# Optimization experiments

Hardware: AMD Instinct MI355X
Metric: run time of the kernel (lower is better)

## Reference

```python
import jax, jax.numpy as jnp
import numpy as np

N_MBED = 384
HEAD_SIZE = 64

def setup_inputs() -> dict:
    key = jax.random.key(0)
    kx, kq, kk, kv = jax.random.split(key, 4)
    B, T = 128, 256
    x = jax.random.normal(kx, (B, T, N_MBED), dtype=jnp.float32)
    # torch nn.Linear(n_mbed, head_size, bias=False): y = x @ W^T, W:[head_size, n_mbed].
    # We store the transposed weight [n_mbed, head_size] so y = x @ W.
    s = 1.0 / np.sqrt(N_MBED)
    Wq = jax.random.uniform(kq, (N_MBED, HEAD_SIZE), jnp.float32, -s, s)
    Wk = jax.random.uniform(kk, (N_MBED, HEAD_SIZE), jnp.float32, -s, s)
    Wv = jax.random.uniform(kv, (N_MBED, HEAD_SIZE), jnp.float32, -s, s)
    return {"x": x, "Wq": Wq, "Wk": Wk, "Wv": Wv}

def reference(x, Wq, Wk, Wv):
    B, T, C = x.shape  # C = n_mbed = 384
    q = x @ Wq  # [B,T,H]
    k = x @ Wk
    v = x @ Wv
    # Faithful to source: wei = k @ q^T, scaled by C**-0.5 (C = n_mbed, not head_size)
    wei = jnp.einsum('bth,bsh->bts', k, q) * (C ** -0.5)  # [B,T,T]
    mask = jnp.tril(jnp.ones((T, T), dtype=bool))
    wei = jnp.where(mask, wei, -jnp.inf)
    wei = jax.nn.softmax(wei, axis=-1)
    # dropout omitted (eval mode / identity)
    out = jnp.einsum('bts,bsh->bth', wei, v)  # [B,T,H]
    return out
```

## Files before the change

### kernel.cpp

```cpp
#include <hip/hip_runtime.h>
#include <hip/hip_bf16.h>
#include <math.h>

constexpr int kB = 128;
constexpr int kT = 256;
constexpr int kC = 384;
constexpr int kH = 64;

using bf16x8 = __attribute__((ext_vector_type(8))) short;
using f32x4  = __attribute__((ext_vector_type(4))) float;

union BF4 { short4 s; __hip_bfloat162 h[2]; };

__device__ inline short4 cvt4(float4 a) {
    BF4 u;
    u.h[0] = __float22bfloat162_rn(float2{a.x, a.y});
    u.h[1] = __float22bfloat162_rn(float2{a.z, a.w});
    return u.s;
}
__device__ inline short bf1(float f) {
    __hip_bfloat16 h = __float2bfloat16(f);
    return *(short*)&h;
}

__global__ void prep_kernel(const float* __restrict__ Wq,
                            const float* __restrict__ Wk,
                            const float* __restrict__ Wv,
                            __hip_bfloat16* __restrict__ Wt) {
    int idx = blockIdx.x * 256 + threadIdx.x;
    int n = idx / kC, c = idx % kC;
    int w = n >> 6, h = n & 63;
    const float* W = (w == 0) ? Wq : (w == 1) ? Wk : Wv;
    float val = W[c * kH + h];
    if (w == 1) val *= 0.051031036307982884f;
    Wt[idx] = __float2bfloat16(val);
}

__global__ __launch_bounds__(256, 4) void proj_kernel(
    const float* __restrict__ x, const __hip_bfloat16* __restrict__ Wt,
    short* __restrict__ Qg, short* __restrict__ Kg, short* __restrict__ VTg)
{
    __shared__ short As[2][64 * 36];
    __shared__ short Bs[2][192 * 36];

    const int bid = blockIdx.x;
    const int b   = bid & 127;
    const int q4  = bid >> 7;
    const int row0 = b * kT + q4 * 64;

    const int tid  = threadIdx.x;
    const int wave = tid >> 6, lane = tid & 63;
    const int m16  = lane & 15, quad = lane >> 4;
    const short* wt = (const short*)Wt;

    const int arow = tid >> 2, acol = (tid & 3) * 8;
    const float* xr = x + (size_t)(row0 + arow) * kC;

    float4 la[2]; bf16x8 lb[3];
    auto glod = [&](int k0) {
        la[0] = *(const float4*)(xr + k0 + acol);
        la[1] = *(const float4*)(xr + k0 + acol + 4);
#pragma unroll
        for (int p = 0; p < 3; ++p) {
            int c = tid + 256 * p, n = c >> 2, kk = (c & 3) * 8;
            lb[p] = *(const bf16x8*)(wt + (size_t)n * kC + k0 + kk);
        }
    };
    auto swr = [&](int d) {
        *(short4*)&As[d][arow * 36 + acol]     = cvt4(la[0]);
        *(short4*)&As[d][arow * 36 + acol + 4] = cvt4(la[1]);
#pragma unroll
        for (int p = 0; p < 3; ++p) {
            int c = tid + 256 * p, n = c >> 2, kk = (c & 3) * 8;
            *(bf16x8*)&Bs[d][n * 36 + kk] = lb[p];
        }
    };

    f32x4 acc[4][3];
#pragma unroll
    for (int mt = 0; mt < 4; ++mt)
#pragma unroll
        for (int j = 0; j < 3; ++j) acc[mt][j] = f32x4{0.f, 0.f, 0.f, 0.f};

    glod(0);
    swr(0);
    __syncthreads();

    for (int s = 0; s < 12; ++s) {
        const int d = s & 1;
        if (s < 11) glod((s + 1) * 32);

        bf16x8 af[4];
#pragma unroll
        for (int mt = 0; mt < 4; ++mt)
            af[mt] = *(const bf16x8*)&As[d][(mt * 16 + m16) * 36 + quad * 8];
#pragma unroll
        for (int j = 0; j < 3; ++j) {
            const bf16x8 bfr =
                *(const bf16x8*)&Bs[d][((wave * 3 + j) * 16 + m16) * 36 + quad * 8];
#pragma unroll
            for (int mt = 0; mt < 4; ++mt)
                acc[mt][j] = __builtin_amdgcn_mfma_f32_16x16x32_bf16(
                    af[mt], bfr, acc[mt][j], 0, 0, 0);
        }

        if (s < 11) swr(d ^ 1);
        __syncthreads();
    }

#pragma unroll
    for (int mt = 0; mt < 4; ++mt) {
        const int mrow = mt * 16 + quad * 4;
#pragma unroll
        for (int j = 0; j < 3; ++j) {
            const int nt = wave * 3 + j;
            const int w  = nt >> 2;
            const int h  = (nt & 3) * 16 + m16;
            if (w == 2) {
                float4 f = make_float4(acc[mt][j][0], acc[mt][j][1],
                                       acc[mt][j][2], acc[mt][j][3]);
                *(short4*)&VTg[((size_t)b * kH + h) * kT + q4 * 64 + mrow] = cvt4(f);
            } else {
                short* G = (w == 1) ? Kg : Qg;
#pragma unroll
                for (int r = 0; r < 4; ++r)
                    G[((size_t)b * kT + q4 * 64 + mrow + r) * kH + h] = bf1(acc[mt][j][r]);
            }
        }
    }
}

__global__ __launch_bounds__(256, 4) void attn_kernel(
    const short* __restrict__ Qg, const short* __restrict__ Kg,
    const short* __restrict__ VTg, float* __restrict__ out)
{
    __shared__ short Pbuf[4][16 * 72];

    const int bid = blockIdx.x;
    const int b   = ((bid >> 5) << 3) | (bid & 7);
    const int qi  = (bid >> 3) & 3;

    const int tid  = threadIdx.x;
    const int wave = tid >> 6, lane = tid & 63;
    const int m16  = lane & 15, quad = lane >> 4;
    const int trow0 = qi * 64 + wave * 16;

    const short* Qb = Qg  + (size_t)b * kT * kH;
    const short* Kb = Kg  + (size_t)b * kT * kH;
    const short* Vb = VTg + (size_t)b * kH * kT;
    short* Pb = Pbuf[wave];

    const bf16x8 ka0 = *(const bf16x8*)&Kb[(trow0 + m16) * kH + quad * 8];
    const bf16x8 ka1 = *(const bf16x8*)&Kb[(trow0 + m16) * kH + quad * 8 + 32];

    f32x4 O[4];
    float m_[4], l_[4];
#pragma unroll
    for (int i = 0; i < 4; ++i) {
        O[i] = f32x4{0.f, 0.f, 0.f, 0.f};
        m_[i] = -INFINITY; l_[i] = 0.f;
    }

    for (int i = 0; i <= qi; ++i) {
        const bool diag = (i == qi);
        const int jmax = diag ? wave : 3;

        f32x4 S[4];
        const f32x4 Z = f32x4{0.f, 0.f, 0.f, 0.f};
#pragma unroll
        for (int j = 0; j < 4; ++j) {
            if (j <= jmax) {
                const int s = i * 64 + j * 16 + m16;
                bf16x8 qb0 = *(const bf16x8*)&Qb[s * kH + quad * 8];
                bf16x8 qb1 = *(const bf16x8*)&Qb[s * kH + quad * 8 + 32];
                S[j] = __builtin_amdgcn_mfma_f32_16x16x32_bf16(ka0, qb0, Z, 0, 0, 0);
                S[j] = __builtin_amdgcn_mfma_f32_16x16x32_bf16(ka1, qb1, S[j], 0, 0, 0);
            }
        }
        if (diag) {
#pragma unroll
            for (int r = 0; r < 4; ++r)
                if (m16 > quad * 4 + r) S[jmax][r] = -INFINITY;
        }

        float P[4][4];
#pragma unroll
        for (int j = 0; j < 4; ++j)
#pragma unroll
            for (int r = 0; r < 4; ++r) P[j][r] = 0.f;
#pragma unroll
        for (int r = 0; r < 4; ++r) {
            float rm = -INFINITY;
#pragma unroll
            for (int j = 0; j < 4; ++j)
                if (j <= jmax) rm = fmaxf(rm, S[j][r]);
            rm = fmaxf(rm, __shfl_xor(rm, 1, 64));
            rm = fmaxf(rm, __shfl_xor(rm, 2, 64));
            rm = fmaxf(rm, __shfl_xor(rm, 4, 64));
            rm = fmaxf(rm, __shfl_xor(rm, 8, 64));
            const float mn = fmaxf(m_[r], rm);
            const float al = __expf(m_[r] - mn);
            m_[r] = mn;
            float rs = 0.f;
#pragma unroll
            for (int j = 0; j < 4; ++j) {
                if (j <= jmax) { P[j][r] = __expf(S[j][r] - mn); rs += P[j][r]; }
            }
            rs += __shfl_xor(rs, 1, 64);
            rs += __shfl_xor(rs, 2, 64);
            rs += __shfl_xor(rs, 4, 64);
            rs += __shfl_xor(rs, 8, 64);
            l_[r] = l_[r] * al + rs;
            O[0][r] *= al; O[1][r] *= al; O[2][r] *= al; O[3][r] *= al;
        }

#pragma unroll
        for (int j = 0; j < 4; ++j)
#pragma unroll
            for (int r = 0; r < 4; ++r)
                Pb[(quad * 4 + r) * 72 + j * 16 + m16] = bf1(P[j][r]);
        bf16x8 pf0 = *(const bf16x8*)&Pb[m16 * 72 + quad * 8];
        bf16x8 pf1 = *(const bf16x8*)&Pb[m16 * 72 + quad * 8 + 32];

#pragma unroll
        for (int ht = 0; ht < 4; ++ht) {
            bf16x8 vb0 = *(const bf16x8*)&Vb[(ht * 16 + m16) * kT + i * 64 + quad * 8];
            bf16x8 vb1 = *(const bf16x8*)&Vb[(ht * 16 + m16) * kT + i * 64 + quad * 8 + 32];
            O[ht] = __builtin_amdgcn_mfma_f32_16x16x32_bf16(pf0, vb0, O[ht], 0, 0, 0);
            O[ht] = __builtin_amdgcn_mfma_f32_16x16x32_bf16(pf1, vb1, O[ht], 0, 0, 0);
        }
    }

#pragma unroll
    for (int r = 0; r < 4; ++r) {
        const float inv = 1.f / l_[r];
        const size_t row = (size_t)(b * kT + trow0 + quad * 4 + r);
#pragma unroll
        for (int ht = 0; ht < 4; ++ht)
            out[row * kH + ht * 16 + m16] = O[ht][r] * inv;
    }
}

extern "C" void kernel_launch(void* const* d_in, const int* in_sizes, int n_in,
                              void* d_out, int out_size, void* d_ws, size_t ws_size,
                              hipStream_t stream) {
    const float* x  = (const float*)d_in[0];
    const float* Wq = (const float*)d_in[1];
    const float* Wk = (const float*)d_in[2];
    const float* Wv = (const float*)d_in[3];
    float* out = (float*)d_out;

    short* base = (short*)d_ws;
    __hip_bfloat16* Wt = (__hip_bfloat16*)base;
    short* Qg  = base + 73728;
    short* Kg  = Qg + (size_t)kB * kT * kH;
    short* VTg = Kg + (size_t)kB * kT * kH;

    prep_kernel<<<(192 * kC) / 256, 256, 0, stream>>>(Wq, Wk, Wv, Wt);
    proj_kernel<<<dim3(512), 256, 0, stream>>>(x, Wt, Qg, Kg, VTg);
    attn_kernel<<<dim3(512), 256, 0, stream>>>(Qg, Kg, VTg, out);
}
```

Before: 122.1 us.

## Transpose QK^T MFMA so softmax rows reduce within lanes, prefetch V

The QK^T MFMA operands are swapped so each lane holds one query row's scores across its four accumulator registers. Row max and row sum then reduce mostly within a lane, with two cross-quad shuffles instead of four shuffles per register, and online-softmax state shrinks to one scalar per lane. The rescale factor and final normalizer are broadcast back to the output layout with shuffles. The P tile is now written as packed bf16 pairs, V fragments are loaded before the QK phase to hide latency, and s_setprio raises wave priority around the MFMA blocks. The layout swap touches the masking, reduction and output paths, so any index mistake would break correctness.

```diff
diff --git a/kernel.cpp b/kernel.cpp
--- a/kernel.cpp
+++ b/kernel.cpp
@@ -154,86 +154,110 @@
     const bf16x8 ka1 = *(const bf16x8*)&Kb[(trow0 + m16) * kH + quad * 8 + 32];
 
     f32x4 O[4];
-    float m_[4], l_[4];
-#pragma unroll
-    for (int i = 0; i < 4; ++i) {
-        O[i] = f32x4{0.f, 0.f, 0.f, 0.f};
-        m_[i] = -INFINITY; l_[i] = 0.f;
-    }
+#pragma unroll
+    for (int i = 0; i < 4; ++i) O[i] = f32x4{0.f, 0.f, 0.f, 0.f};
+    float m_ = -INFINITY, l_ = 0.f;
 
     for (int i = 0; i <= qi; ++i) {
         const bool diag = (i == qi);
         const int jmax = diag ? wave : 3;
 
+        bf16x8 vb[4][2];
+#pragma unroll
+        for (int ht = 0; ht < 4; ++ht) {
+            vb[ht][0] = *(const bf16x8*)&Vb[(ht * 16 + m16) * kT + i * 64 + quad * 8];
+            vb[ht][1] = *(const bf16x8*)&Vb[(ht * 16 + m16) * kT + i * 64 + quad * 8 + 32];
+        }
+
         f32x4 S[4];
         const f32x4 Z = f32x4{0.f, 0.f, 0.f, 0.f};
+        __builtin_amdgcn_s_setprio(1);
 #pragma unroll
         for (int j = 0; j < 4; ++j) {
             if (j <= jmax) {
                 const int s = i * 64 + j * 16 + m16;
                 bf16x8 qb0 = *(const bf16x8*)&Qb[s * kH + quad * 8];
                 bf16x8 qb1 = *(const bf16x8*)&Qb[s * kH + quad * 8 + 32];
-                S[j] = __builtin_amdgcn_mfma_f32_16x16x32_bf16(ka0, qb0, Z, 0, 0, 0);
-                S[j] = __builtin_amdgcn_mfma_f32_16x16x32_bf16(ka1, qb1, S[j], 0, 0, 0);
-            }
-        }
+                S[j] = __builtin_amdgcn_mfma_f32_16x16x32_bf16(qb0, ka0, Z, 0, 0, 0);
+                S[j] = __builtin_amdgcn_mfma_f32_16x16x32_bf16(qb1, ka1, S[j], 0, 0, 0);
+            }
+        }
+        __builtin_amdgcn_s_setprio(0);
         if (diag) {
 #pragma unroll
             for (int r = 0; r < 4; ++r)
-                if (m16 > quad * 4 + r) S[jmax][r] = -INFINITY;
-        }
+                if (quad * 4 + r > m16) S[jmax][r] = -INFINITY;
+        }
+
+        float rm = -INFINITY;
+#pragma unroll
+        for (int j = 0; j < 4; ++j)
+            if (j <= jmax)
+#pragma unroll
+                for (int r = 0; r < 4; ++r) rm = fmaxf(rm, S[j][r]);
+        rm = fmaxf(rm, __shfl_xor(rm, 16, 64));
+        rm = fmaxf(rm, __shfl_xor(rm, 32, 64));
+
+        const float mn = fmaxf(m_, rm);
+        const float al = __expf(m_ - mn);
+        m_ = mn;
 
         float P[4][4];
 #pragma unroll
         for (int j = 0; j < 4; ++j)
 #pragma unroll
             for (int r = 0; r < 4; ++r) P[j][r] = 0.f;
-#pragma unroll
-        for (int r = 0; r < 4; ++r) {
-            float rm = -INFINITY;
-#pragma unroll
-            for (int j = 0; j < 4; ++j)
-                if (j <= jmax) rm = fmaxf(rm, S[j][r]);
-            rm = fmaxf(rm, __shfl_xor(rm, 1, 64));
-            rm = fmaxf(rm, __shfl_xor(rm, 2, 64));
-            rm = fmaxf(rm, __shfl_xor(rm, 4, 64));
-            rm = fmaxf(rm, __shfl_xor(rm, 8, 64));
-            const float mn = fmaxf(m_[r], rm);
-            const float al = __expf(m_[r] - mn);
-            m_[r] = mn;
-            float rs = 0.f;
-#pragma unroll
-            for (int j = 0; j < 4; ++j) {
-                if (j <= jmax) { P[j][r] = __expf(S[j][r] - mn); rs += P[j][r]; }
-            }
-            rs += __shfl_xor(rs, 1, 64);
-            rs += __shfl_xor(rs, 2, 64);
-            rs += __shfl_xor(rs, 4, 64);
-            rs += __shfl_xor(rs, 8, 64);
-            l_[r] = l_[r] * al + rs;
-            O[0][r] *= al; O[1][r] *= al; O[2][r] *= al; O[3][r] *= al;
-        }
+        float rs = 0.f;
+#pragma unroll
+        for (int j = 0; j < 4; ++j) {
+            if (j <= jmax) {
+#pragma unroll
+                for (int r = 0; r < 4; ++r) {
+                    P[j][r] = __expf(S[j][r] - mn);
+                    rs += P[j][r];
+                }
+            }
+        }
+        rs += __shfl_xor(rs, 16, 64);
+        rs += __shfl_xor(rs, 32, 64);
+        l_ = l_ * al + rs;
+
+        float albc[4];
+#pragma unroll
+        for (int r = 0; r < 4; ++r)
+            albc[r] = __shfl(al, (quad << 4) | (quad * 4 + r), 64);
+#pragma unroll
+        for (int ht = 0; ht < 4; ++ht)
+#pragma unroll
+            for (int r = 0; r < 4; ++r) O[ht][r] *= albc[r];
 
 #pragma unroll
         for (int j = 0; j < 4; ++j)
 #pragma unroll
-            for (int r = 0; r < 4; ++r)
-                Pb[(quad * 4 + r) * 72 + j * 16 + m16] = bf1(P[j][r]);
+            for (int p = 0; p < 2; ++p) {
+                __hip_bfloat162 w =
+                    __float22bfloat162_rn(float2{P[j][2 * p], P[j][2 * p + 1]});
+                *(__hip_bfloat162*)&Pb[m16 * 72 + j * 16 + quad * 4 + 2 * p] = w;
+            }
         bf16x8 pf0 = *(const bf16x8*)&Pb[m16 * 72 + quad * 8];
         bf16x8 pf1 = *(const bf16x8*)&Pb[m16 * 72 + quad * 8 + 32];
 
+        __builtin_amdgcn_s_setprio(1);
 #pragma unroll
         for (int ht = 0; ht < 4; ++ht) {
-            bf16x8 vb0 = *(const bf16x8*)&Vb[(ht * 16 + m16) * kT + i * 64 + quad * 8];
-            bf16x8 vb1 = *(const bf16x8*)&Vb[(ht * 16 + m16) * kT + i * 64 + quad * 8 + 32];
-            O[ht] = __builtin_amdgcn_mfma_f32_16x16x32_bf16(pf0, vb0, O[ht], 0, 0, 0);
-            O[ht] = __builtin_amdgcn_mfma_f32_16x16x32_bf16(pf1, vb1, O[ht], 0, 0, 0);
-        }
-    }
-
+            O[ht] = __builtin_amdgcn_mfma_f32_16x16x32_bf16(pf0, vb[ht][0], O[ht], 0, 0, 0);
+            O[ht] = __builtin_amdgcn_mfma_f32_16x16x32_bf16(pf1, vb[ht][1], O[ht], 0, 0, 0);
+        }
+        __builtin_amdgcn_s_setprio(0);
+    }
+
+    float lbc[4];
+#pragma unroll
+    for (int r = 0; r < 4; ++r)
+        lbc[r] = __shfl(l_, (quad << 4) | (quad * 4 + r), 64);
 #pragma unroll
     for (int r = 0; r < 4; ++r) {
-        const float inv = 1.f / l_[r];
+        const float inv = 1.f / lbc[r];
         const size_t row = (size_t)(b * kT + trow0 + quad * 4 + r);
 #pragma unroll
         for (int ht = 0; ht < 4; ++ht)
```

Result: no change. 122.4 us (+0.2%).
